# Performance work log

Measured on AMD Instinct MI355X. Metric: run time of the kernel, lower is better.

The kernel has to match this reference:

```python
import jax, jax.numpy as jnp
import numpy as np
from jax import lax

N = 31      # perfect binary tree, root = node 0, children of i are 2i+1, 2i+2
CH = 10     # hidden channels (out_channel)
S = 8       # hidden spatial size = h_list // 4


def conv3d(x, w, b=None, pad=1):
    out = lax.conv_general_dilated(
        x, w, window_strides=(1, 1, 1), padding=[(pad, pad)] * 3,
        dimension_numbers=('NCDHW', 'OIDHW', 'NCDHW'))
    if b is not None:
        out = out + b[None, :, None, None, None]
    return out


def maxpool2(x):
    return lax.reduce_window(x, -jnp.inf, lax.max, (1, 1, 2, 2, 2), (1, 1, 2, 2, 2), 'VALID')


def up2(x):  # nearest-neighbor upsample x2 on D,H,W
    return jnp.repeat(jnp.repeat(jnp.repeat(x, 2, axis=2), 2, axis=3), 2, axis=4)


def setup_inputs() -> dict:
    key = jax.random.key(0)
    ks = iter(jax.random.split(key, 32))
    r = lambda shape, s=0.1: jax.random.normal(next(ks), shape, dtype=jnp.float32) * s
    inp = {
        'data': jax.random.normal(next(ks), (N, 1, 32, 32, 32), dtype=jnp.float32),
        'h0': jnp.zeros((N, CH, S, S, S), jnp.float32),
        'c0': jnp.zeros((N, CH, S, S, S), jnp.float32),
        'e1a_w': r((16, 1, 3, 3, 3)), 'e1a_b': jnp.zeros((16,), jnp.float32),
        'e1b_w': r((16, 16, 3, 3, 3)), 'e1b_b': jnp.zeros((16,), jnp.float32),
        'e2a_w': r((32, 16, 3, 3, 3)), 'e2a_b': jnp.zeros((32,), jnp.float32),
        'e2b_w': r((20, 32, 3, 3, 3)), 'e2b_b': jnp.zeros((20,), jnp.float32),
        'd2a_w': r((20, 30, 3, 3, 3)), 'd2a_b': jnp.zeros((20,), jnp.float32),
        'd2b_w': r((32, 20, 3, 3, 3)), 'd2b_b': jnp.zeros((32,), jnp.float32),
        'd1a_w': r((16, 48, 3, 3, 3)), 'd1a_b': jnp.zeros((16,), jnp.float32),
        'd1b_w': r((16, 16, 3, 3, 3)), 'd1b_b': jnp.zeros((16,), jnp.float32),
        'd1c_w': r((1, 16, 1, 1, 1)), 'd1c_b': jnp.zeros((1,), jnp.float32),
        'w_iou': r((30, 20, 3, 3, 3)),
        'u_iou': r((30, 10, 3, 3, 3)),
        'u_f': r((10, 10, 3, 3, 3)),
        'b_iou': jnp.zeros((30, S, S, S), jnp.float32),
    }
    return inp


def reference(data, h0, c0, e1a_w, e1a_b, e1b_w, e1b_b, e2a_w, e2a_b, e2b_w, e2b_b,
              d2a_w, d2a_b, d2b_w, d2b_b, d1a_w, d1a_b, d1b_w, d1b_b, d1c_w, d1c_b,
              w_iou, u_iou, u_f, b_iou):
    relu = jax.nn.relu
    # ---- Encoder ----
    x0 = relu(conv3d(relu(conv3d(data, e1a_w, e1a_b)), e1b_w, e1b_b))   # [N,16,32,32,32]
    x = maxpool2(x0)
    x1 = relu(conv3d(relu(conv3d(x, e2a_w, e2a_b)), e2b_w, e2b_b))      # [N,20,16,16,16]
    x = maxpool2(x1)                                                    # [N,20,8,8,8]
    Wx = conv3d(x, w_iou)                                               # [N,30,8,8,8]

    h_all = jnp.zeros((N, CH, S, S, S), Wx.dtype)
    c_all = jnp.zeros((N, CH, S, S, S), Wx.dtype)

    def apply_node(iou, c_in):
        i, o, u = jnp.split(iou + b_iou, 3, axis=1)
        c = jax.nn.sigmoid(i) * jnp.tanh(u) + c_in
        h = jax.nn.sigmoid(o) * jnp.tanh(c)
        return h, c

    # ---- leaves (no children): iou = W_iou(x), c term = initial c0 ----
    leaf = np.arange(N // 2, N)
    h, c = apply_node(Wx[leaf], c0[leaf])
    h_all = h_all.at[leaf].set(h)
    c_all = c_all.at[leaf].set(c)

    # ---- internal levels, bottom-up (topological propagation) ----
    depth = int(np.log2(N + 1))  # 5
    for lvl in range(depth - 2, -1, -1):
        idx = np.arange(2 ** lvl - 1, 2 ** (lvl + 1) - 1)
        ch = np.stack([2 * idx + 1, 2 * idx + 2], axis=1)  # [P,2] children indices
        P = idx.shape[0]
        h_ch = h_all[ch]                                   # [P,2,CH,S,S,S]
        c_ch = c_all[ch]
        h_sum = h_ch.sum(axis=1)
        f = jax.nn.sigmoid(conv3d(h_ch.reshape(P * 2, CH, S, S, S), u_f)).reshape(h_ch.shape)
        c_red = (f * c_ch).sum(axis=1)
        iou = conv3d(h_sum, u_iou)  # NOTE: overwrites W_iou(x) for internal nodes (as in source)
        h, c = apply_node(iou, c_red)
        h_all = h_all.at[idx].set(h)
        c_all = c_all.at[idx].set(c)

    # ---- Decoder (Dropout = identity in eval) ----
    y = up2(h_all)                      # [N,10,16,16,16]
    y = jnp.concatenate([y, x1], axis=1)  # 30 ch
    y = relu(conv3d(y, d2a_w, d2a_b))
    y = relu(conv3d(y, d2b_w, d2b_b))   # 32 ch
    y = up2(y)
    y = jnp.concatenate([y, x0], axis=1)  # 48 ch
    y = relu(conv3d(y, d1a_w, d1a_b))
    y = relu(conv3d(y, d1b_w, d1b_b))
    y = conv3d(y, d1c_w, d1c_b, pad=0)  # [N,1,32,32,32]
    return y
```

## Files before the change

### kernel.cpp

```cpp
#include <hip/hip_runtime.h>
#include <math.h>

typedef _Float16 h2 __attribute__((ext_vector_type(2)));
typedef _Float16 half4_t __attribute__((ext_vector_type(4)));
typedef float f32x4 __attribute__((ext_vector_type(4)));

__device__ inline h2 uph(unsigned u) { return __builtin_bit_cast(h2, u); }
__device__ inline unsigned pkh(float a, float b) {
    return __builtin_bit_cast(unsigned, __builtin_amdgcn_cvt_pkrtz(a, b));
}
__device__ inline float sigf(float x) { return 1.f / (1.f + expf(-x)); }

__global__ __launch_bounds__(256) void repackall(
    const float* __restrict__ s0, const float* __restrict__ s1,
    const float* __restrict__ s2, const float* __restrict__ s3,
    const float* __restrict__ s4, const float* __restrict__ s5,
    const float* __restrict__ s6, const float* __restrict__ s7,
    const float* __restrict__ s8, const float* __restrict__ s9,
    _Float16* __restrict__ dst)
{
    int t = blockIdx.x * 256 + threadIdx.x;
    if (t >= 179712) return;
    const int offs[11] = {0, 6912, 20736, 48384, 76032, 103680, 124416,
                          131328, 158976, 172800, 179712};
    const int ciwA[10] = {16, 16, 32, 30, 20, 48, 16, 20, 10, 10};
    const int coA[10]  = {16, 32, 20, 20, 32, 16, 16, 30, 30, 10};
    const int nchA[10] = {1, 1, 2, 2, 2, 3, 1, 2, 1, 1};
    int seg = 0;
    while (t >= offs[seg + 1]) ++seg;
    int lt = t - offs[seg];
    const float* src = seg == 0 ? s0 : seg == 1 ? s1 : seg == 2 ? s2 :
                       seg == 3 ? s3 : seg == 4 ? s4 : seg == 5 ? s5 :
                       seg == 6 ? s6 : seg == 7 ? s7 : seg == 8 ? s8 : s9;
    int CIw = ciwA[seg], CO = coA[seg], NCH = nchA[seg];
    int cip = lt & 15, co = (lt >> 4) & 15, r = lt >> 8;
    int tap = r % 27, rc = r / 27;
    int chunk = rc % NCH, slab = rc / NCH;
    int slot_l = ((cip >> 2) - (co >> 2)) & 3;
    int gci = chunk * 16 + slot_l * 4 + (cip & 3);
    int gco = slab * 16 + co;
    float v = 0.f;
    if (gci < CIw && gco < CO) v = src[((size_t)gco * CIw + gci) * 27 + tap];
    dst[t] = (_Float16)v;
}

template<int NCH, int UPP, int UP2, int S2, bool FUSE>
__global__ __launch_bounds__(256) void conv3m(
    const _Float16* __restrict__ up, const _Float16* __restrict__ src,
    const _Float16* __restrict__ bwg, const float* __restrict__ bias,
    _Float16* __restrict__ out, const float* __restrict__ w1c,
    const float* __restrict__ b1c, float* __restrict__ out32)
{
    constexpr int ROWS = 10, COLS = 34;
    constexpr int NG   = 3 * ROWS * COLS * 2;
    constexpr int ITERS = 8;

    __shared__ __align__(16) _Float16 win[3 * ROWS * COLS * 16];
    __shared__ __align__(16) _Float16 bw[6912];

    const int tid  = threadIdx.x;
    const int lane = tid & 63;
    const int wv   = tid >> 6;
    const int l16  = lane & 15;
    const int quad = lane >> 4;

    const int h0 = (blockIdx.x & 3) * 8;
    const int d  = (blockIdx.x >> 2) & 31;
    const int n  = blockIdx.x >> 7;

    size_t baseU[ITERS], baseS[ITERS];
    int dA[ITERS], dB[ITERS];
    bool vld[ITERS];
#pragma unroll
    for (int it = 0; it < ITERS; ++it) {
        int t = tid + it * 256;
        vld[it] = false; dA[it] = 0; dB[it] = 0; baseU[it] = 0; baseS[it] = 0;
        if (t < NG) {
            int g   = t & 1;
            int idx = t >> 1;
            int cc  = idx % COLS;
            int rr  = idx / COLS;
            int hh  = rr % ROWS;
            int dp  = rr / ROWS;
            int zd = d - 1 + dp, zh = h0 + hh - 1, zw = cc - 1;
            vld[it] = (unsigned)zd < 32u && (unsigned)zh < 32u && (unsigned)zw < 32u;
            int rot  = (cc >> 2) & 3;
            int cell = (rr * COLS + cc) * 16;
            dA[it] = cell + (((2 * g + rot) & 3) << 2);
            dB[it] = cell + (((2 * g + 1 + rot) & 3) << 2);
            if (vld[it]) {
                if (UPP > 0)
                    baseU[it] = ((((size_t)n * 16 + (zd >> 1)) * 16 + (zh >> 1)) * 16
                                 + (zw >> 1)) * UP2 + g * 8;
                baseS[it] = ((((size_t)n * 32 + zd) * 32 + zh) * 32 + zw) * S2 + g * 8;
            }
        }
    }

    f32x4 acc[4];
    {
        float b0 = bias[l16];
#pragma unroll
        for (int i = 0; i < 4; ++i) acc[i] = f32x4{b0, b0, b0, b0};
    }

    const int brot = ((quad + (l16 >> 2)) & 3) << 2;

    uint4 preA[ITERS];
    uint4 preB[4];

    auto loadA = [&](int cib) {
        const int cb = cib * 16;
        const bool isup = (UPP > 0) && (cb < UPP);
#pragma unroll
        for (int it = 0; it < ITERS; ++it) {
            int t = tid + it * 256;
            uint4 v = uint4{0u, 0u, 0u, 0u};
            if (t < NG && vld[it]) {
                const _Float16* pp = isup ? (up + baseU[it] + cb)
                                          : (src + baseS[it] + (cb - UPP));
                v = *(const uint4*)pp;
            }
            preA[it] = v;
        }
    };
    auto loadB = [&](int cib) {
        const uint4* bsrc = (const uint4*)(bwg + (size_t)cib * 6912);
#pragma unroll
        for (int it = 0; it < 4; ++it) {
            int t = tid + it * 256;
            preB[it] = (t < 864) ? bsrc[t] : uint4{0u, 0u, 0u, 0u};
        }
    };

    loadA(0);
    loadB(0);

#pragma unroll
    for (int cib = 0; cib < NCH; ++cib) {
        if (cib) __syncthreads();
#pragma unroll
        for (int it = 0; it < 4; ++it) {
            int t = tid + it * 256;
            if (t < 864) ((uint4*)bw)[t] = preB[it];
        }
#pragma unroll
        for (int it = 0; it < ITERS; ++it) {
            int t = tid + it * 256;
            if (t < NG) {
                *(uint2*)&win[dA[it]] = make_uint2(preA[it].x, preA[it].y);
                *(uint2*)&win[dB[it]] = make_uint2(preA[it].z, preA[it].w);
            }
        }
        if (cib + 1 < NCH) { loadA(cib + 1); loadB(cib + 1); }
        __syncthreads();

#pragma unroll
        for (int kd = 0; kd < 3; ++kd) {
#pragma unroll
            for (int kw = 0; kw < 3; ++kw) {
                half4_t bf[3];
#pragma unroll
                for (int kh = 0; kh < 3; ++kh)
                    bf[kh] = *(const half4_t*)&bw[((kd * 3 + kh) * 3 + kw) * 256 + l16 * 16 + brot];
                half4_t af[2][4];
#pragma unroll
                for (int p = 0; p < 2; ++p) {
                    const int ww = p * 16 + l16 + kw;
                    const int arot = ((quad + (ww >> 2)) & 3) << 2;
#pragma unroll
                    for (int rr = 0; rr < 4; ++rr) {
                        const int row = kd * ROWS + wv * 2 + rr;
                        af[p][rr] = *(const half4_t*)&win[(row * COLS + ww) * 16 + arot];
                    }
                }
#pragma unroll
                for (int kh = 0; kh < 3; ++kh)
#pragma unroll
                    for (int i = 0; i < 4; ++i)
                        acc[i] = __builtin_amdgcn_mfma_f32_16x16x16f16(
                            af[i & 1][(i >> 1) + kh], bf[kh], acc[i], 0, 0, 0);
            }
        }
    }

    if (FUSE) {
        const float wc = w1c[l16];
        const float bb = b1c[0];
#pragma unroll
        for (int i = 0; i < 4; ++i) {
            const int h = h0 + wv * 2 + (i >> 1);
            const int wb0 = (i & 1) * 16;
#pragma unroll
            for (int r = 0; r < 4; ++r) {
                float v = fmaxf(acc[i][r], 0.f) * wc;
                v += __shfl_xor(v, 1);
                v += __shfl_xor(v, 2);
                v += __shfl_xor(v, 4);
                v += __shfl_xor(v, 8);
                if (l16 == 0) {
                    const int w = wb0 + quad * 4 + r;
                    out32[(((size_t)n * 32 + d) * 32 + h) * 32 + w] = v + bb;
                }
            }
        }
    } else {
#pragma unroll
        for (int i = 0; i < 4; ++i) {
            const int h = h0 + wv * 2 + (i >> 1);
            const int wb0 = (i & 1) * 16;
#pragma unroll
            for (int r = 0; r < 4; ++r) {
                const int w = wb0 + quad * 4 + r;
                size_t sp = (((size_t)n * 32 + d) * 32 + h) * 32 + w;
                out[sp * 16 + l16] = (_Float16)fmaxf(acc[i][r], 0.f);
            }
        }
    }
}

template<int NCH, int NSLAB, int S2, int CO>
__global__ __launch_bounds__(256) void conv3m16(
    const _Float16* __restrict__ src, const _Float16* __restrict__ bwg,
    const float* __restrict__ bias, _Float16* __restrict__ out)
{
    constexpr int ROWS = 18, COLS = 18;
    constexpr int CELLS = 3 * ROWS * COLS;
    constexpr int ITERS = 4;

    __shared__ __align__(16) _Float16 win[CELLS * 16];
    __shared__ __align__(16) _Float16 bw[NSLAB * 6912];

    const int tid  = threadIdx.x;
    const int lane = tid & 63;
    const int wv   = tid >> 6;
    const int l16  = lane & 15;
    const int quad = lane >> 4;

    const int d = blockIdx.x & 15;
    const int n = blockIdx.x >> 4;

    unsigned baseS[ITERS], pk[ITERS];
    bool vld[ITERS];
#pragma unroll
    for (int it = 0; it < ITERS; ++it) {
        int t = tid + it * 256;
        vld[it] = false; baseS[it] = 0; pk[it] = 0;
        if (t < CELLS) {
            int cc = t % COLS, rr = t / COLS;
            int hh = rr % ROWS, dp = rr / ROWS;
            int zd = d - 1 + dp, zh = hh - 1, zw = cc - 1;
            vld[it] = (unsigned)zd < 16u && (unsigned)zh < 16u && (unsigned)zw < 16u;
            pk[it] = (unsigned)(t * 16) | ((unsigned)((cc >> 2) & 3) << 28);
            if (vld[it])
                baseS[it] = (unsigned)((((n * 16 + zd) * 16 + zh) * 16 + zw) * S2);
        }
    }

    f32x4 acc[NSLAB][4];
#pragma unroll
    for (int s = 0; s < NSLAB; ++s) {
        int cg = s * 16 + l16;
        float b0 = (cg < CO) ? bias[cg] : 0.f;
#pragma unroll
        for (int i = 0; i < 4; ++i) acc[s][i] = f32x4{b0, b0, b0, b0};
    }
    const int brot = ((quad + (l16 >> 2)) & 3) << 2;

    uint4 preA0[ITERS], preA1[ITERS], preB[NSLAB][4];

    auto loadA = [&](int cib) {
        const int cb = cib * 16;
#pragma unroll
        for (int it = 0; it < ITERS; ++it) {
            uint4 v0 = uint4{0u, 0u, 0u, 0u}, v1 = v0;
            int t = tid + it * 256;
            if (t < CELLS && vld[it]) {
                const _Float16* p = src + baseS[it] + cb;
                v0 = *(const uint4*)p;
                v1 = *(const uint4*)(p + 8);
            }
            preA0[it] = v0; preA1[it] = v1;
        }
    };
    auto loadB = [&](int cib) {
#pragma unroll
        for (int s = 0; s < NSLAB; ++s) {
            const uint4* bsrc = (const uint4*)(bwg + (size_t)(s * NCH + cib) * 6912);
#pragma unroll
            for (int it = 0; it < 4; ++it) {
                int t = tid + it * 256;
                preB[s][it] = (t < 864) ? bsrc[t] : uint4{0u, 0u, 0u, 0u};
            }
        }
    };

    loadA(0);
    loadB(0);

#pragma unroll
    for (int cib = 0; cib < NCH; ++cib) {
        if (cib) __syncthreads();
#pragma unroll
        for (int s = 0; s < NSLAB; ++s)
#pragma unroll
            for (int it = 0; it < 4; ++it) {
                int t = tid + it * 256;
                if (t < 864) ((uint4*)(bw + s * 6912))[t] = preB[s][it];
            }
#pragma unroll
        for (int it = 0; it < ITERS; ++it) {
            int t = tid + it * 256;
            if (t < CELLS) {
                int cell = pk[it] & 0x0FFFFFFF;
                int rot  = pk[it] >> 28;
                *(uint2*)&win[cell + (((rot + 0) & 3) << 2)] = make_uint2(preA0[it].x, preA0[it].y);
                *(uint2*)&win[cell + (((rot + 1) & 3) << 2)] = make_uint2(preA0[it].z, preA0[it].w);
                *(uint2*)&win[cell + (((rot + 2) & 3) << 2)] = make_uint2(preA1[it].x, preA1[it].y);
                *(uint2*)&win[cell + (((rot + 3) & 3) << 2)] = make_uint2(preA1[it].z, preA1[it].w);
            }
        }
        if (cib + 1 < NCH) { loadA(cib + 1); loadB(cib + 1); }
        __syncthreads();

#pragma unroll
        for (int kd = 0; kd < 3; ++kd) {
#pragma unroll
            for (int kw = 0; kw < 3; ++kw) {
                half4_t af[6];
                const int ww = l16 + kw;
                const int arot = ((quad + (ww >> 2)) & 3) << 2;
#pragma unroll
                for (int rr = 0; rr < 6; ++rr) {
                    const int row = kd * ROWS + wv * 4 + rr;
                    af[rr] = *(const half4_t*)&win[(row * COLS + ww) * 16 + arot];
                }
#pragma unroll
                for (int kh = 0; kh < 3; ++kh) {
                    const int tap = (kd * 3 + kh) * 3 + kw;
#pragma unroll
                    for (int s = 0; s < NSLAB; ++s) {
                        half4_t bf = *(const half4_t*)&bw[s * 6912 + tap * 256 + l16 * 16 + brot];
#pragma unroll
                        for (int i = 0; i < 4; ++i)
                            acc[s][i] = __builtin_amdgcn_mfma_f32_16x16x16f16(
                                af[i + kh], bf, acc[s][i], 0, 0, 0);
                    }
                }
            }
        }
    }

#pragma unroll
    for (int s = 0; s < NSLAB; ++s) {
        int cg = s * 16 + l16;
        if (cg < CO) {
#pragma unroll
            for (int i = 0; i < 4; ++i) {
                const int h = wv * 4 + i;
#pragma unroll
                for (int r = 0; r < 4; ++r) {
                    const int w = quad * 4 + r;
                    size_t sp = (((size_t)n * 16 + d) * 16 + h) * 16 + w;
                    out[sp * 32 + cg] = (_Float16)fmaxf(acc[s][i][r], 0.f);
                }
            }
        }
    }
}

__global__ __launch_bounds__(256) void conv3e1a(
    const float* __restrict__ src, const float* __restrict__ wgt,
    const float* __restrict__ bias, _Float16* __restrict__ out)
{
    __shared__ float sw[27 * 16];
    const int tid = threadIdx.x;
    const int wq = tid % 8;
    const int h  = (tid / 8) % 32;
    const int w0 = wq * 4;
    const int n  = blockIdx.x / 32;
    const int d  = blockIdx.x % 32;

    for (int t = tid; t < 27 * 16; t += 256) {
        int co = t % 16, tap = t / 16;
        sw[t] = wgt[(size_t)co * 27 + tap];
    }
    __syncthreads();

    float acc[16][4];
#pragma unroll
    for (int co = 0; co < 16; ++co) {
        float b0 = bias[co];
        acc[co][0] = b0; acc[co][1] = b0; acc[co][2] = b0; acc[co][3] = b0;
    }

#pragma unroll
    for (int kd = 0; kd < 3; ++kd) {
        int zd = d + kd - 1;
        if ((unsigned)zd >= 32u) continue;
#pragma unroll
        for (int kh = 0; kh < 3; ++kh) {
            int zh = h + kh - 1;
            if ((unsigned)zh >= 32u) continue;
            const float* p = src + ((size_t)n * 32 + zd) * 1024 + zh * 32;
            float v[6];
#pragma unroll
            for (int j = 0; j < 6; ++j) {
                int zw = w0 - 1 + j;
                v[j] = ((unsigned)zw < 32u) ? p[zw] : 0.f;
            }
            const float* swp = &sw[(kd * 9 + kh * 3) * 16];
#pragma unroll
            for (int kw = 0; kw < 3; ++kw)
#pragma unroll
                for (int co = 0; co < 16; ++co)
#pragma unroll
                    for (int j = 0; j < 4; ++j)
                        acc[co][j] = fmaf(v[kw + j], swp[kw * 16 + co], acc[co][j]);
        }
    }

#pragma unroll
    for (int j = 0; j < 4; ++j) {
        unsigned u[8];
#pragma unroll
        for (int cp = 0; cp < 8; ++cp)
            u[cp] = pkh(fmaxf(acc[2 * cp][j], 0.f), fmaxf(acc[2 * cp + 1][j], 0.f));
        _Float16* base = out + ((((size_t)n * 32 + d) * 32 + h) * 32 + (w0 + j)) * 16;
        *(uint4*)base       = make_uint4(u[0], u[1], u[2], u[3]);
        *(uint4*)(base + 8) = make_uint4(u[4], u[5], u[6], u[7]);
    }
}

__global__ __launch_bounds__(256) void maxpool16(
    const unsigned* __restrict__ in, unsigned* __restrict__ out, int total)
{
    int t = blockIdx.x * 256 + threadIdx.x;
    if (t >= total) return;
    int cp = t & 7, w = (t >> 3) & 15, h = (t >> 7) & 15, d = (t >> 11) & 15, n = t >> 15;
    float m0 = -1e30f, m1 = -1e30f;
#pragma unroll
    for (int a = 0; a < 2; ++a)
#pragma unroll
        for (int b = 0; b < 2; ++b)
#pragma unroll
            for (int c = 0; c < 2; ++c) {
                size_t sp = (((size_t)n * 32 + 2 * d + a) * 32 + 2 * h + b) * 32 + 2 * w + c;
                h2 x = uph(in[sp * 8 + cp]);
                m0 = fmaxf(m0, (float)x.x);
                m1 = fmaxf(m1, (float)x.y);
            }
    out[(((size_t)(n * 16 + d) * 16 + h) * 16 + w) * 8 + cp] = pkh(m0, m1);
}

__global__ __launch_bounds__(256) void poolx1(
    const unsigned* __restrict__ x1u, unsigned* __restrict__ out, int total)
{
    int t = blockIdx.x * 256 + threadIdx.x;
    if (t >= total) return;
    int cp = t & 15, s = (t >> 4) & 511, n = t >> 13;
    int w = s & 7, h = (s >> 3) & 7, d = s >> 6;
    unsigned o = 0u;
    if (cp < 10) {
        float m0 = -1e30f, m1 = -1e30f;
#pragma unroll
        for (int a = 0; a < 2; ++a)
#pragma unroll
            for (int b = 0; b < 2; ++b)
#pragma unroll
                for (int c = 0; c < 2; ++c) {
                    size_t sp = (((size_t)n * 16 + 2 * d + a) * 16 + 2 * h + b) * 16 + 2 * w + c;
                    h2 x = uph(x1u[sp * 16 + cp]);
                    m0 = fmaxf(m0, (float)x.x);
                    m1 = fmaxf(m1, (float)x.y);
                }
        o = pkh(m0, m1);
    }
    out[((size_t)n * 512 + s) * 16 + cp] = o;
}

__global__ __launch_bounds__(256) void catk(
    const unsigned* __restrict__ h_allu, const unsigned* __restrict__ x1u,
    unsigned* __restrict__ cat1u, int total)
{
    int t = blockIdx.x * 256 + threadIdx.x;
    if (t >= total) return;
    int cp = t & 15, ww = (t >> 4) & 15, hh = (t >> 8) & 15, dd = (t >> 12) & 15, n = t >> 16;
    unsigned v = 0u;
    if (cp < 5) {
        int sph = (dd >> 1) * 64 + (hh >> 1) * 8 + (ww >> 1);
        v = h_allu[((size_t)n * 512 + sph) * 8 + cp];
    } else if (cp < 15) {
        v = x1u[((((size_t)n * 16 + dd) * 16 + hh) * 16 + ww) * 16 + (cp - 5)];
    }
    cat1u[t] = v;
}

__global__ __launch_bounds__(256) void treeleafM(
    const _Float16* __restrict__ xp2, const _Float16* __restrict__ bwio,
    const float* __restrict__ b_iou, const float* __restrict__ c0,
    _Float16* __restrict__ h_all, _Float16* __restrict__ c_all)
{
    __shared__ __align__(16) _Float16 buf[16384];
    __shared__ __align__(16) _Float16 bw[13824];
    const int tid = threadIdx.x, lane = tid & 63, wv = tid >> 6;
    const int l16 = lane & 15, quad = lane >> 4;
    const int node = 15 + blockIdx.x;
    const _Float16* xb = xp2 + (size_t)node * 512 * 32;
    const int brot = ((quad + (l16 >> 2)) & 3) << 2;

    int base[8];
#pragma unroll
    for (int i = 0; i < 8; ++i) {
        int s = (wv * 8 + i) * 16 + l16;
        base[i] = ((s >> 6) * 10 + ((s >> 3) & 7)) * 10 + (s & 7);
    }

    f32x4 acc[2][8];
#pragma unroll
    for (int sl = 0; sl < 2; ++sl)
#pragma unroll
        for (int i = 0; i < 8; ++i) acc[sl][i] = f32x4{0.f, 0.f, 0.f, 0.f};

    for (int ck = 0; ck < 2; ++ck) {
        if (ck) __syncthreads();
        {
            const uint4* s0 = (const uint4*)(bwio + (size_t)(0 * 2 + ck) * 6912);
            const uint4* s1 = (const uint4*)(bwio + (size_t)(1 * 2 + ck) * 6912);
#pragma unroll
            for (int it = 0; it < 4; ++it) {
                int t = tid + it * 256;
                if (t < 864) { ((uint4*)bw)[t] = s0[t]; ((uint4*)(bw + 6912))[t] = s1[t]; }
            }
        }
#pragma unroll
        for (int it = 0; it < 8; ++it) {
            int t = tid + it * 256;
            if (t < 2000) {
                int g = t & 1, c = t >> 1;
                int zw = c % 10, r = c / 10, zh = r % 10, zd = r / 10;
                int d = zd - 1, h = zh - 1, w = zw - 1;
                uint4 v = uint4{0u, 0u, 0u, 0u};
                if ((unsigned)d < 8u && (unsigned)h < 8u && (unsigned)w < 8u)
                    v = *(const uint4*)(xb + ((d * 8 + h) * 8 + w) * 32 + ck * 16 + g * 8);
                int rot = (c >> 2) & 3;
                *(uint2*)&buf[c * 16 + (((2 * g + rot) & 3) << 2)]     = make_uint2(v.x, v.y);
                *(uint2*)&buf[c * 16 + (((2 * g + 1 + rot) & 3) << 2)] = make_uint2(v.z, v.w);
            }
        }
        __syncthreads();

        for (int kd = 0; kd < 3; ++kd)
        for (int kh = 0; kh < 3; ++kh)
#pragma unroll
        for (int kw = 0; kw < 3; ++kw) {
            int tap = (kd * 3 + kh) * 3 + kw, toff = kd * 100 + kh * 10 + kw;
            half4_t bf0 = *(const half4_t*)&bw[tap * 256 + l16 * 16 + brot];
            half4_t bf1 = *(const half4_t*)&bw[6912 + tap * 256 + l16 * 16 + brot];
#pragma unroll
            for (int i = 0; i < 8; ++i) {
                int cell = base[i] + toff;
                int arot = ((quad + ((cell >> 2) & 3)) & 3) << 2;
                half4_t af = *(const half4_t*)&buf[cell * 16 + arot];
                acc[0][i] = __builtin_amdgcn_mfma_f32_16x16x16f16(af, bf0, acc[0][i], 0, 0, 0);
                acc[1][i] = __builtin_amdgcn_mfma_f32_16x16x16f16(af, bf1, acc[1][i], 0, 0, 0);
            }
        }
    }
    __syncthreads();
#pragma unroll
    for (int sl = 0; sl < 2; ++sl)
#pragma unroll
        for (int i = 0; i < 8; ++i)
#pragma unroll
            for (int r = 0; r < 4; ++r) {
                int s = (wv * 8 + i) * 16 + quad * 4 + r;
                buf[s * 32 + sl * 16 + l16] = (_Float16)acc[sl][i][r];
            }
    __syncthreads();
    for (int sl2 = 0; sl2 < 2; ++sl2) {
        int s = tid + sl2 * 256;
        const uint4* ip = (const uint4*)&buf[s * 32];
        uint4 q0 = ip[0], q1 = ip[1], q2 = ip[2], q3 = ip[3];
        unsigned uw[16] = {q0.x, q0.y, q0.z, q0.w, q1.x, q1.y, q1.z, q1.w,
                           q2.x, q2.y, q2.z, q2.w, q3.x, q3.y, q3.z, q3.w};
        float io[32];
#pragma unroll
        for (int k = 0; k < 16; ++k) { h2 p = uph(uw[k]); io[2 * k] = (float)p.x; io[2 * k + 1] = (float)p.y; }
        unsigned hp[8], cp[8];
#pragma unroll
        for (int q = 0; q < 5; ++q) {
            float hn[2], cn[2];
#pragma unroll
            for (int e = 0; e < 2; ++e) {
                int chn = 2 * q + e;
                float iv = io[chn]      + b_iou[(size_t)chn * 512 + s];
                float ov = io[10 + chn] + b_iou[(size_t)(10 + chn) * 512 + s];
                float uv = io[20 + chn] + b_iou[(size_t)(20 + chn) * 512 + s];
                float cin = c0[((size_t)node * 10 + chn) * 512 + s];
                cn[e] = sigf(iv) * tanhf(uv) + cin;
                hn[e] = sigf(ov) * tanhf(cn[e]);
            }
            hp[q] = pkh(hn[0], hn[1]);
            cp[q] = pkh(cn[0], cn[1]);
        }
        hp[5] = hp[6] = hp[7] = 0u; cp[5] = cp[6] = cp[7] = 0u;
        uint4* ho = (uint4*)(h_all + ((size_t)node * 512 + s) * 16);
        uint4* co_ = (uint4*)(c_all + ((size_t)node * 512 + s) * 16);
        ho[0] = make_uint4(hp[0], hp[1], hp[2], hp[3]);
        ho[1] = make_uint4(hp[4], hp[5], hp[6], hp[7]);
        co_[0] = make_uint4(cp[0], cp[1], cp[2], cp[3]);
        co_[1] = make_uint4(cp[4], cp[5], cp[6], cp[7]);
    }
}

__global__ __launch_bounds__(256) void treelevelM(
    const _Float16* __restrict__ bwuf, const _Float16* __restrict__ bwui,
    const float* __restrict__ b_iou,
    _Float16* __restrict__ h_all, _Float16* __restrict__ c_all,
    int pb, int cb)
{
    __shared__ __align__(16) _Float16 buf[16384];
    __shared__ __align__(16) _Float16 bw[13824];
    const int tid = threadIdx.x, lane = tid & 63, wv = tid >> 6;
    const int l16 = lane & 15, quad = lane >> 4;
    const int node = pb + blockIdx.x;
    const int c0n = cb + 2 * blockIdx.x;
    const int brot = ((quad + (l16 >> 2)) & 3) << 2;

    int base[8];
#pragma unroll
    for (int i = 0; i < 8; ++i) {
        int s = (wv * 8 + i) * 16 + l16;
        base[i] = ((s >> 6) * 10 + ((s >> 3) & 7)) * 10 + (s & 7);
    }

    float cred[10][2];
#pragma unroll
    for (int c = 0; c < 10; ++c) cred[c][0] = cred[c][1] = 0.f;

#pragma unroll
    for (int it = 0; it < 4; ++it) {
        int t = tid + it * 256;
        if (t < 864) ((uint4*)bw)[t] = ((const uint4*)bwuf)[t];
    }

    for (int e = 0; e < 2; ++e) {
        const _Float16* hb = h_all + (size_t)(c0n + e) * 512 * 16;
        if (e) __syncthreads();
#pragma unroll
        for (int it = 0; it < 8; ++it) {
            int t = tid + it * 256;
            if (t < 2000) {
                int g = t & 1, c = t >> 1;
                int zw = c % 10, r = c / 10, zh = r % 10, zd = r / 10;
                int d = zd - 1, h = zh - 1, w = zw - 1;
                uint4 v = uint4{0u, 0u, 0u, 0u};
                if ((unsigned)d < 8u && (unsigned)h < 8u && (unsigned)w < 8u)
                    v = *(const uint4*)(hb + ((d * 8 + h) * 8 + w) * 16 + g * 8);
                int rot = (c >> 2) & 3;
                *(uint2*)&buf[c * 16 + (((2 * g + rot) & 3) << 2)]     = make_uint2(v.x, v.y);
                *(uint2*)&buf[c * 16 + (((2 * g + 1 + rot) & 3) << 2)] = make_uint2(v.z, v.w);
            }
        }
        __syncthreads();
        f32x4 accf[8];
#pragma unroll
        for (int i = 0; i < 8; ++i) accf[i] = f32x4{0.f, 0.f, 0.f, 0.f};
        for (int kd = 0; kd < 3; ++kd)
        for (int kh = 0; kh < 3; ++kh)
#pragma unroll
        for (int kw = 0; kw < 3; ++kw) {
            int tap = (kd * 3 + kh) * 3 + kw, toff = kd * 100 + kh * 10 + kw;
            half4_t bf = *(const half4_t*)&bw[tap * 256 + l16 * 16 + brot];
#pragma unroll
            for (int i = 0; i < 8; ++i) {
                int cell = base[i] + toff;
                int arot = ((quad + ((cell >> 2) & 3)) & 3) << 2;
                half4_t af = *(const half4_t*)&buf[cell * 16 + arot];
                accf[i] = __builtin_amdgcn_mfma_f32_16x16x16f16(af, bf, accf[i], 0, 0, 0);
            }
        }
        __syncthreads();
#pragma unroll
        for (int i = 0; i < 8; ++i)
#pragma unroll
            for (int r = 0; r < 4; ++r) {
                int s = (wv * 8 + i) * 16 + quad * 4 + r;
                buf[s * 16 + l16] = (_Float16)accf[i][r];
            }
        __syncthreads();
        for (int sl2 = 0; sl2 < 2; ++sl2) {
            int s = tid + sl2 * 256;
            const uint4* fp_ = (const uint4*)&buf[s * 16];
            uint4 f0 = fp_[0], f1 = fp_[1];
            unsigned fw[8] = {f0.x, f0.y, f0.z, f0.w, f1.x, f1.y, f1.z, f1.w};
            const uint4* cc = (const uint4*)(c_all + ((size_t)(c0n + e) * 512 + s) * 16);
            uint4 c0v = cc[0], c1v = cc[1];
            unsigned cw[8] = {c0v.x, c0v.y, c0v.z, c0v.w, c1v.x, c1v.y, c1v.z, c1v.w};
#pragma unroll
            for (int q = 0; q < 5; ++q) {
                h2 fv = uph(fw[q]); h2 cv = uph(cw[q]);
                cred[2 * q][sl2]     += sigf((float)fv.x) * (float)cv.x;
                cred[2 * q + 1][sl2] += sigf((float)fv.y) * (float)cv.y;
            }
        }
    }
    __syncthreads();
#pragma unroll
    for (int it = 0; it < 7; ++it) {
        int t = tid + it * 256;
        if (t < 1728) ((uint4*)bw)[t] = ((const uint4*)bwui)[t];
    }
    {
        const _Float16* h0b = h_all + (size_t)c0n * 512 * 16;
        const _Float16* h1b = h_all + (size_t)(c0n + 1) * 512 * 16;
#pragma unroll
        for (int it = 0; it < 8; ++it) {
            int t = tid + it * 256;
            if (t < 2000) {
                int g = t & 1, c = t >> 1;
                int zw = c % 10, r = c / 10, zh = r % 10, zd = r / 10;
                int d = zd - 1, h = zh - 1, w = zw - 1;
                uint4 v = uint4{0u, 0u, 0u, 0u};
                if ((unsigned)d < 8u && (unsigned)h < 8u && (unsigned)w < 8u) {
                    size_t off = ((d * 8 + h) * 8 + w) * 16 + g * 8;
                    uint4 a = *(const uint4*)(h0b + off);
                    uint4 b = *(const uint4*)(h1b + off);
                    unsigned* av = &a.x; unsigned* bv = &b.x; unsigned* vv = &v.x;
#pragma unroll
                    for (int k = 0; k < 4; ++k) {
                        h2 x = uph(av[k]); h2 y = uph(bv[k]);
                        vv[k] = pkh((float)x.x + (float)y.x, (float)x.y + (float)y.y);
                    }
                }
                int rot = (c >> 2) & 3;
                *(uint2*)&buf[c * 16 + (((2 * g + rot) & 3) << 2)]     = make_uint2(v.x, v.y);
                *(uint2*)&buf[c * 16 + (((2 * g + 1 + rot) & 3) << 2)] = make_uint2(v.z, v.w);
            }
        }
    }
    __syncthreads();
    f32x4 acc[2][8];
#pragma unroll
    for (int sl = 0; sl < 2; ++sl)
#pragma unroll
        for (int i = 0; i < 8; ++i) acc[sl][i] = f32x4{0.f, 0.f, 0.f, 0.f};
    for (int kd = 0; kd < 3; ++kd)
    for (int kh = 0; kh < 3; ++kh)
#pragma unroll
    for (int kw = 0; kw < 3; ++kw) {
        int tap = (kd * 3 + kh) * 3 + kw, toff = kd * 100 + kh * 10 + kw;
        half4_t bf0 = *(const half4_t*)&bw[tap * 256 + l16 * 16 + brot];
        half4_t bf1 = *(const half4_t*)&bw[6912 + tap * 256 + l16 * 16 + brot];
#pragma unroll
        for (int i = 0; i < 8; ++i) {
            int cell = base[i] + toff;
            int arot = ((quad + ((cell >> 2) & 3)) & 3) << 2;
            half4_t af = *(const half4_t*)&buf[cell * 16 + arot];
            acc[0][i] = __builtin_amdgcn_mfma_f32_16x16x16f16(af, bf0, acc[0][i], 0, 0, 0);
            acc[1][i] = __builtin_amdgcn_mfma_f32_16x16x16f16(af, bf1, acc[1][i], 0, 0, 0);
        }
    }
    __syncthreads();
#pragma unroll
    for (int sl = 0; sl < 2; ++sl)
#pragma unroll
        for (int i = 0; i < 8; ++i)
#pragma unroll
            for (int r = 0; r < 4; ++r) {
                int s = (wv * 8 + i) * 16 + quad * 4 + r;
                buf[s * 32 + sl * 16 + l16] = (_Float16)acc[sl][i][r];
            }
    __syncthreads();
    for (int sl2 = 0; sl2 < 2; ++sl2) {
        int s = tid + sl2 * 256;
        const uint4* ip = (const uint4*)&buf[s * 32];
        uint4 q0 = ip[0], q1 = ip[1], q2 = ip[2], q3 = ip[3];
        unsigned uw[16] = {q0.x, q0.y, q0.z, q0.w, q1.x, q1.y, q1.z, q1.w,
                           q2.x, q2.y, q2.z, q2.w, q3.x, q3.y, q3.z, q3.w};
        float io[32];
#pragma unroll
        for (int k = 0; k < 16; ++k) { h2 p = uph(uw[k]); io[2 * k] = (float)p.x; io[2 * k + 1] = (float)p.y; }
        unsigned hp[8], cp[8];
#pragma unroll
        for (int q = 0; q < 5; ++q) {
            float hn[2], cn[2];
#pragma unroll
            for (int e = 0; e < 2; ++e) {
                int chn = 2 * q + e;
                float iv = io[chn]      + b_iou[(size_t)chn * 512 + s];
                float ov = io[10 + chn] + b_iou[(size_t)(10 + chn) * 512 + s];
                float uv = io[20 + chn] + b_iou[(size_t)(20 + chn) * 512 + s];
                cn[e] = sigf(iv) * tanhf(uv) + cred[chn][sl2];
                hn[e] = sigf(ov) * tanhf(cn[e]);
            }
            hp[q] = pkh(hn[0], hn[1]);
            cp[q] = pkh(cn[0], cn[1]);
        }
        hp[5] = hp[6] = hp[7] = 0u; cp[5] = cp[6] = cp[7] = 0u;
        uint4* ho = (uint4*)(h_all + ((size_t)node * 512 + s) * 16);
        uint4* co_ = (uint4*)(c_all + ((size_t)node * 512 + s) * 16);
        ho[0] = make_uint4(hp[0], hp[1], hp[2], hp[3]);
        ho[1] = make_uint4(hp[4], hp[5], hp[6], hp[7]);
        co_[0] = make_uint4(cp[0], cp[1], cp[2], cp[3]);
        co_[1] = make_uint4(cp[4], cp[5], cp[6], cp[7]);
    }
}

extern "C" void kernel_launch(void* const* d_in, const int* in_sizes, int n_in,
                              void* d_out, int out_size, void* d_ws, size_t ws_size,
                              hipStream_t stream)
{
    const float* data  = (const float*)d_in[0];
    const float* c0    = (const float*)d_in[2];
    const float* e1a_w = (const float*)d_in[3];  const float* e1a_b = (const float*)d_in[4];
    const float* e1b_w = (const float*)d_in[5];  const float* e1b_b = (const float*)d_in[6];
    const float* e2a_w = (const float*)d_in[7];  const float* e2a_b = (const float*)d_in[8];
    const float* e2b_w = (const float*)d_in[9];  const float* e2b_b = (const float*)d_in[10];
    const float* d2a_w = (const float*)d_in[11]; const float* d2a_b = (const float*)d_in[12];
    const float* d2b_w = (const float*)d_in[13]; const float* d2b_b = (const float*)d_in[14];
    const float* d1a_w = (const float*)d_in[15]; const float* d1a_b = (const float*)d_in[16];
    const float* d1b_w = (const float*)d_in[17]; const float* d1b_b = (const float*)d_in[18];
    const float* d1c_w = (const float*)d_in[19]; const float* d1c_b = (const float*)d_in[20];
    const float* w_iou = (const float*)d_in[21];
    const float* u_iou = (const float*)d_in[22];
    const float* u_f   = (const float*)d_in[23];
    const float* b_iou = (const float*)d_in[24];

    unsigned* ws = (unsigned*)d_ws;
    size_t o = 0;
    unsigned* t1u   = ws + o; o += 8126464;
    unsigned* x0u   = ws + o; o += 8126464;
    unsigned* xpu   = ws + o; o += 1015808;
    unsigned* t2u   = ws + o; o += 2031616;
    unsigned* x1u   = ws + o; o += 2031616;
    unsigned* cat1u = ws + o; o += 2031616;
    unsigned* y2u   = ws + o; o += 2031616;
    unsigned* xp2u  = ws + o; o += 253952;
    unsigned* h_allu= ws + o; o += 126976;
    unsigned* c_allu= ws + o; o += 126976;
    unsigned* bwgu  = ws + o; o += 89856;
    (void)ws_size; (void)in_sizes; (void)n_in; (void)out_size;

    _Float16* t1h  = (_Float16*)t1u;
    _Float16* x0h  = (_Float16*)x0u;
    _Float16* xph  = (_Float16*)xpu;
    _Float16* t2h  = (_Float16*)t2u;
    _Float16* x1h  = (_Float16*)x1u;
    _Float16* cath = (_Float16*)cat1u;
    _Float16* y2h  = (_Float16*)y2u;
    _Float16* xp2h = (_Float16*)xp2u;
    _Float16* h_allh = (_Float16*)h_allu;
    _Float16* c_allh = (_Float16*)c_allu;
    _Float16* t3h  = t2h;
    _Float16* t4h  = t1h;
    _Float16* bwg  = (_Float16*)bwgu;

    _Float16* b_e1b = bwg;
    _Float16* b_e2a = bwg + 6912;
    _Float16* b_e2b = bwg + 20736;
    _Float16* b_d2a = bwg + 48384;
    _Float16* b_d2b = bwg + 76032;
    _Float16* b_d1a = bwg + 103680;
    _Float16* b_d1b = bwg + 124416;
    _Float16* b_wio = bwg + 131328;
    _Float16* b_uio = bwg + 158976;
    _Float16* b_uf  = bwg + 172800;

    dim3 b256(256);

    repackall<<<dim3(702), b256, 0, stream>>>(
        e1b_w, e2a_w, e2b_w, d2a_w, d2b_w, d1a_w, d1b_w, w_iou, u_iou, u_f, bwg);

    conv3e1a<<<dim3(992), b256, 0, stream>>>(data, e1a_w, e1a_b, t1h);
    conv3m<1, 0, 0, 16, false><<<dim3(3968), b256, 0, stream>>>(
        nullptr, t1h, b_e1b, e1b_b, x0h, nullptr, nullptr, nullptr);
    maxpool16<<<dim3(3968), b256, 0, stream>>>(x0u, xpu, 1015808);
    conv3m16<1, 2, 16, 32><<<dim3(496), b256, 0, stream>>>(xph, b_e2a, e2a_b, t2h);
    conv3m16<2, 2, 32, 20><<<dim3(496), b256, 0, stream>>>(t2h, b_e2b, e2b_b, x1h);
    poolx1<<<dim3(992), b256, 0, stream>>>(x1u, xp2u, 253952);

    treeleafM<<<dim3(16), b256, 0, stream>>>(xp2h, b_wio, b_iou, c0, h_allh, c_allh);
    for (int lvl = 3; lvl >= 0; --lvl) {
        int P = 1 << lvl;
        treelevelM<<<dim3(P), b256, 0, stream>>>(
            b_uf, b_uio, b_iou, h_allh, c_allh, P - 1, 2 * P - 1);
    }

    catk<<<dim3(7936), b256, 0, stream>>>(h_allu, x1u, cat1u, 2031616);
    conv3m16<2, 2, 32, 20><<<dim3(496), b256, 0, stream>>>(cath, b_d2a, d2a_b, t3h);
    conv3m16<2, 2, 32, 32><<<dim3(496), b256, 0, stream>>>(t3h, b_d2b, d2b_b, y2h);
    conv3m<3, 32, 32, 16, false><<<dim3(3968), b256, 0, stream>>>(
        y2h, x0h, b_d1a, d1a_b, t4h, nullptr, nullptr, nullptr);
    conv3m<1, 0, 0, 16, true><<<dim3(3968), b256, 0, stream>>>(
        nullptr, t4h, b_d1b, d1b_b, nullptr, d1c_w, d1c_b, (float*)d_out);
}
```

Before: 525.0 us.

## Keep single-chunk conv weights in registers; write e2b output directly into concat buffer

For the single-chunk 32^3 convolutions, each lane loads its 27 weight fragments straight into registers. This drops the shared-memory weight staging and shrinks LDS use, which may allow more resident blocks. Separately, the e2b conv now writes its output into the concat buffer at channel offset 10. The old concat kernel is replaced by an upfill kernel that only writes the upsampled tree channels plus the zero-pad slot, and the pooling kernel reads from the concat buffer. This saves one full buffer copy and a workspace allocation, at the cost of 27 extra half4 registers per thread.

```diff
diff --git a/kernel.cpp b/kernel.cpp
--- a/kernel.cpp
+++ b/kernel.cpp
@@ -44,7 +44,7 @@
     dst[t] = (_Float16)v;
 }
 
-template<int NCH, int UPP, int UP2, int S2, bool FUSE>
+template<int NCH, int UPP, int UP2, int S2, bool FUSE, bool REGB>
 __global__ __launch_bounds__(256) void conv3m(
     const _Float16* __restrict__ up, const _Float16* __restrict__ src,
     const _Float16* __restrict__ bwg, const float* __restrict__ bias,
@@ -56,7 +56,7 @@
     constexpr int ITERS = 8;
 
     __shared__ __align__(16) _Float16 win[3 * ROWS * COLS * 16];
-    __shared__ __align__(16) _Float16 bw[6912];
+    __shared__ __align__(16) _Float16 bw[REGB ? 16 : 6912];
 
     const int tid  = threadIdx.x;
     const int lane = tid & 63;
@@ -67,6 +67,15 @@
     const int h0 = (blockIdx.x & 3) * 8;
     const int d  = (blockIdx.x >> 2) & 31;
     const int n  = blockIdx.x >> 7;
+
+    const int brot = ((quad + (l16 >> 2)) & 3) << 2;
+
+    half4_t breg[REGB ? 27 : 1];
+    if (REGB) {
+#pragma unroll
+        for (int tap = 0; tap < 27; ++tap)
+            breg[tap] = *(const half4_t*)(bwg + tap * 256 + l16 * 16 + brot);
+    }
 
     size_t baseU[ITERS], baseS[ITERS];
     int dA[ITERS], dB[ITERS];
@@ -104,8 +113,6 @@
         for (int i = 0; i < 4; ++i) acc[i] = f32x4{b0, b0, b0, b0};
     }
 
-    const int brot = ((quad + (l16 >> 2)) & 3) << 2;
-
     uint4 preA[ITERS];
     uint4 preB[4];
 
@@ -125,6 +132,7 @@
         }
     };
     auto loadB = [&](int cib) {
+        if (REGB) return;
         const uint4* bsrc = (const uint4*)(bwg + (size_t)cib * 6912);
 #pragma unroll
         for (int it = 0; it < 4; ++it) {
@@ -139,10 +147,12 @@
 #pragma unroll
     for (int cib = 0; cib < NCH; ++cib) {
         if (cib) __syncthreads();
-#pragma unroll
-        for (int it = 0; it < 4; ++it) {
-            int t = tid + it * 256;
-            if (t < 864) ((uint4*)bw)[t] = preB[it];
+        if (!REGB) {
+#pragma unroll
+            for (int it = 0; it < 4; ++it) {
+                int t = tid + it * 256;
+                if (t < 864) ((uint4*)bw)[t] = preB[it];
+            }
         }
 #pragma unroll
         for (int it = 0; it < ITERS; ++it) {
@@ -161,8 +171,11 @@
             for (int kw = 0; kw < 3; ++kw) {
                 half4_t bf[3];
 #pragma unroll
-                for (int kh = 0; kh < 3; ++kh)
-                    bf[kh] = *(const half4_t*)&bw[((kd * 3 + kh) * 3 + kw) * 256 + l16 * 16 + brot];
+                for (int kh = 0; kh < 3; ++kh) {
+                    const int tap = (kd * 3 + kh) * 3 + kw;
+                    bf[kh] = REGB ? breg[tap]
+                                  : *(const half4_t*)&bw[tap * 256 + l16 * 16 + brot];
+                }
                 half4_t af[2][4];
 #pragma unroll
                 for (int p = 0; p < 2; ++p) {
@@ -219,7 +232,7 @@
     }
 }
 
-template<int NCH, int NSLAB, int S2, int CO>
+template<int NCH, int NSLAB, int S2, int CO, int COFF>
 __global__ __launch_bounds__(256) void conv3m16(
     const _Float16* __restrict__ src, const _Float16* __restrict__ bwg,
     const float* __restrict__ bias, _Float16* __restrict__ out)
@@ -362,7 +375,7 @@
                 for (int r = 0; r < 4; ++r) {
                     const int w = quad * 4 + r;
                     size_t sp = (((size_t)n * 16 + d) * 16 + h) * 16 + w;
-                    out[sp * 32 + cg] = (_Float16)fmaxf(acc[s][i][r], 0.f);
+                    out[sp * 32 + COFF + cg] = (_Float16)fmaxf(acc[s][i][r], 0.f);
                 }
             }
         }
@@ -454,7 +467,7 @@
 }
 
 __global__ __launch_bounds__(256) void poolx1(
-    const unsigned* __restrict__ x1u, unsigned* __restrict__ out, int total)
+    const unsigned* __restrict__ catu, unsigned* __restrict__ out, int total)
 {
     int t = blockIdx.x * 256 + threadIdx.x;
     if (t >= total) return;
@@ -470,7 +483,7 @@
 #pragma unroll
                 for (int c = 0; c < 2; ++c) {
                     size_t sp = (((size_t)n * 16 + 2 * d + a) * 16 + 2 * h + b) * 16 + 2 * w + c;
-                    h2 x = uph(x1u[sp * 16 + cp]);
+                    h2 x = uph(catu[sp * 16 + 5 + cp]);
                     m0 = fmaxf(m0, (float)x.x);
                     m1 = fmaxf(m1, (float)x.y);
                 }
@@ -479,21 +492,22 @@
     out[((size_t)n * 512 + s) * 16 + cp] = o;
 }
 
-__global__ __launch_bounds__(256) void catk(
-    const unsigned* __restrict__ h_allu, const unsigned* __restrict__ x1u,
-    unsigned* __restrict__ cat1u, int total)
+__global__ __launch_bounds__(256) void upfill(
+    const unsigned* __restrict__ h_allu, unsigned* __restrict__ catu, int total)
 {
     int t = blockIdx.x * 256 + threadIdx.x;
     if (t >= total) return;
-    int cp = t & 15, ww = (t >> 4) & 15, hh = (t >> 8) & 15, dd = (t >> 12) & 15, n = t >> 16;
+    int cp6 = t % 6, r = t / 6;
+    int sp = r & 4095, n = r >> 12;
     unsigned v = 0u;
-    if (cp < 5) {
+    int cp = 15;
+    if (cp6 < 5) {
+        cp = cp6;
+        int ww = sp & 15, hh = (sp >> 4) & 15, dd = sp >> 8;
         int sph = (dd >> 1) * 64 + (hh >> 1) * 8 + (ww >> 1);
-        v = h_allu[((size_t)n * 512 + sph) * 8 + cp];
-    } else if (cp < 15) {
-        v = x1u[((((size_t)n * 16 + dd) * 16 + hh) * 16 + ww) * 16 + (cp - 5)];
-    }
-    cat1u[t] = v;
+        v = h_allu[((size_t)n * 512 + sph) * 8 + cp6];
+    }
+    catu[((size_t)n * 4096 + sp) * 16 + cp] = v;
 }
 
 __global__ __launch_bounds__(256) void treeleafM(
@@ -834,7 +848,6 @@
     unsigned* x0u   = ws + o; o += 8126464;
     unsigned* xpu   = ws + o; o += 1015808;
     unsigned* t2u   = ws + o; o += 2031616;
-    unsigned* x1u   = ws + o; o += 2031616;
     unsigned* cat1u = ws + o; o += 2031616;
     unsigned* y2u   = ws + o; o += 2031616;
     unsigned* xp2u  = ws + o; o += 253952;
@@ -847,7 +860,6 @@
     _Float16* x0h  = (_Float16*)x0u;
     _Float16* xph  = (_Float16*)xpu;
     _Float16* t2h  = (_Float16*)t2u;
-    _Float16* x1h  = (_Float16*)x1u;
     _Float16* cath = (_Float16*)cat1u;
     _Float16* y2h  = (_Float16*)y2u;
     _Float16* xp2h = (_Float16*)xp2u;
@@ -874,12 +886,12 @@
         e1b_w, e2a_w, e2b_w, d2a_w, d2b_w, d1a_w, d1b_w, w_iou, u_iou, u_f, bwg);
 
     conv3e1a<<<dim3(992), b256, 0, stream>>>(data, e1a_w, e1a_b, t1h);
-    conv3m<1, 0, 0, 16, false><<<dim3(3968), b256, 0, stream>>>(
+    conv3m<1, 0, 0, 16, false, true><<<dim3(3968), b256, 0, stream>>>(
         nullptr, t1h, b_e1b, e1b_b, x0h, nullptr, nullptr, nullptr);
     maxpool16<<<dim3(3968), b256, 0, stream>>>(x0u, xpu, 1015808);
-    conv3m16<1, 2, 16, 32><<<dim3(496), b256, 0, stream>>>(xph, b_e2a, e2a_b, t2h);
-    conv3m16<2, 2, 32, 20><<<dim3(496), b256, 0, stream>>>(t2h, b_e2b, e2b_b, x1h);
-    poolx1<<<dim3(992), b256, 0, stream>>>(x1u, xp2u, 253952);
+    conv3m16<1, 2, 16, 32, 0><<<dim3(496), b256, 0, stream>>>(xph, b_e2a, e2a_b, t2h);
+    conv3m16<2, 2, 32, 20, 10><<<dim3(496), b256, 0, stream>>>(t2h, b_e2b, e2b_b, cath);
+    poolx1<<<dim3(992), b256, 0, stream>>>(cat1u, xp2u, 253952);
 
     treeleafM<<<dim3(16), b256, 0, stream>>>(xp2h, b_wio, b_iou, c0, h_allh, c_allh);
     for (int lvl = 3; lvl >= 0; --lvl) {
@@ -888,11 +900,11 @@
             b_uf, b_uio, b_iou, h_allh, c_allh, P - 1, 2 * P - 1);
     }
 
-    catk<<<dim3(7936), b256, 0, stream>>>(h_allu, x1u, cat1u, 2031616);
-    conv3m16<2, 2, 32, 20><<<dim3(496), b256, 0, stream>>>(cath, b_d2a, d2a_b, t3h);
-    conv3m16<2, 2, 32, 32><<<dim3(496), b256, 0, stream>>>(t3h, b_d2b, d2b_b, y2h);
-    conv3m<3, 32, 32, 16, false><<<dim3(3968), b256, 0, stream>>>(
+    upfill<<<dim3(2976), b256, 0, stream>>>(h_allu, cat1u, 31 * 4096 * 6);
+    conv3m16<2, 2, 32, 20, 0><<<dim3(496), b256, 0, stream>>>(cath, b_d2a, d2a_b, t3h);
+    conv3m16<2, 2, 32, 32, 0><<<dim3(496), b256, 0, stream>>>(t3h, b_d2b, d2b_b, y2h);
+    conv3m<3, 32, 32, 16, false, false><<<dim3(3968), b256, 0, stream>>>(
         y2h, x0h, b_d1a, d1a_b, t4h, nullptr, nullptr, nullptr);
-    conv3m<1, 0, 0, 16, true><<<dim3(3968), b256, 0, stream>>>(
+    conv3m<1, 0, 0, 16, true, true><<<dim3(3968), b256, 0, stream>>>(
         nullptr, t4h, b_d1b, d1b_b, nullptr, d1c_w, d1c_b, (float*)d_out);
 }
```

New measurement: 528.2 us. Within noise of the previous version (+0.6%).
